# Optimization experiments

Measured on AMD Instinct MI355X. Metric: run time of the kernel, lower is better.

Reference implementation:

```python
import jax, jax.numpy as jnp
import numpy as np

D_MODEL = 512


def setup_inputs() -> dict:
    key = jax.random.key(0)
    ks = jax.random.split(key, 5)
    B, S, D = 4, 4096, D_MODEL
    scale = 1.0 / np.sqrt(D)
    return {
        "x": jax.random.normal(ks[0], (B, S, D), dtype=jnp.float32),
        "W_q": jax.random.normal(ks[1], (D, D), dtype=jnp.float32) * scale,
        "W_k": jax.random.normal(ks[2], (D, D), dtype=jnp.float32) * scale,
        "W_v": jax.random.normal(ks[3], (D, D), dtype=jnp.float32) * scale,
        "W_o": jax.random.normal(ks[4], (D, D), dtype=jnp.float32) * scale,
    }


def reference(x, W_q, W_k, W_v, W_o):
    # torch nn.Linear(d,d,bias=False): y = x @ W.T
    q = jnp.einsum("bsd,ed->bse", x, W_q)
    k = jnp.einsum("bsd,ed->bse", x, W_k)
    v = jnp.einsum("bsd,ed->bse", x, W_v)
    d_k = jnp.sqrt(jnp.asarray(D_MODEL, dtype=x.dtype))
    scores = jnp.einsum("bqd,bkd->bqk", q, k) / d_k  # [B,S,S]
    S = scores.shape[-1]
    causal = jnp.tril(jnp.ones((S, S), dtype=bool))  # True where allowed
    scores = jnp.where(causal, scores, -jnp.inf)
    attn = jax.nn.softmax(scores, axis=-1)
    context = jnp.einsum("bqk,bkd->bqd", attn, v)
    return jnp.einsum("bsd,ed->bse", context, W_o)
```

## Files before the change

### kernel.cpp

```cpp
#include <hip/hip_runtime.h>
#include <cstdint>

typedef __attribute__((ext_vector_type(8))) __bf16 bf16x8;
typedef __attribute__((ext_vector_type(4))) float f32x4;
typedef __attribute__((ext_vector_type(8))) unsigned short u16x8;

#define SEQ 4096
#define QKV_LD 1536

__device__ __forceinline__ unsigned short f2bf(float f) {
  unsigned u = __builtin_bit_cast(unsigned, f);
  u += 0x7fffu + ((u >> 16) & 1u);
  return (unsigned short)(u >> 16);
}

__device__ __forceinline__ float bf2f(unsigned short h) {
  return __builtin_bit_cast(float, (unsigned)h << 16);
}

__device__ __forceinline__ void async_copy16(const void* g, const void* lds) {
  __builtin_amdgcn_global_load_lds(
      (const __attribute__((address_space(1))) void*)(uintptr_t)g,
      (__attribute__((address_space(3))) void*)(unsigned)(uintptr_t)lds,
      16, 0, 0);
}

__global__ void cvt_bf16(const float* __restrict__ src, unsigned short* __restrict__ dst, int n) {
  int i = (blockIdx.x * 256 + threadIdx.x) * 4;
  if (i >= n) return;
  float4 v = *(const float4*)(src + i);
  ushort4 o;
  o.x = f2bf(v.x); o.y = f2bf(v.y); o.z = f2bf(v.z); o.w = f2bf(v.w);
  *(ushort4*)(dst + i) = o;
}

template <bool F32OUT>
__global__ __launch_bounds__(256, 2) void gemm_bt(
    const unsigned short* __restrict__ A, const unsigned short* __restrict__ B,
    void* __restrict__ C, int ldc)
{
  __shared__ unsigned short As[128 * 32];
  __shared__ unsigned short Bs[128 * 32];
  const int tid = threadIdx.x;
  const int lane = tid & 63;
  const int w = tid >> 6;
  const int l15 = lane & 15, quad = lane >> 4;
  const int wm = w & 1, wn = w >> 1;
  const long m0 = (long)blockIdx.x * 128;
  const long n0 = (long)blockIdx.y * 128;

  f32x4 acc[4][4] = {};

  for (int kt = 0; kt < 16; ++kt) {
    __syncthreads();
    {
      int c = tid;
      int row = c >> 2, chl = c & 3;
      int gch = (chl - (row >> 1)) & 3;
      async_copy16(A + (m0 + row) * 512 + kt * 32 + gch * 8, As + c * 8);
      async_copy16(B + (n0 + row) * 512 + kt * 32 + gch * 8, Bs + c * 8);
      c = tid + 256;
      row = c >> 2; chl = c & 3;
      gch = (chl - (row >> 1)) & 3;
      async_copy16(A + (m0 + row) * 512 + kt * 32 + gch * 8, As + c * 8);
      async_copy16(B + (n0 + row) * 512 + kt * 32 + gch * 8, Bs + c * 8);
    }
    __syncthreads();

    bf16x8 af[4], bfr[4];
#pragma unroll
    for (int mt = 0; mt < 4; ++mt) {
      int row = wm * 64 + mt * 16 + l15;
      int chl = (quad + (row >> 1)) & 3;
      af[mt] = *(const bf16x8*)(As + row * 32 + chl * 8);
    }
#pragma unroll
    for (int nt = 0; nt < 4; ++nt) {
      int row = wn * 64 + nt * 16 + l15;
      int chl = (quad + (row >> 1)) & 3;
      bfr[nt] = *(const bf16x8*)(Bs + row * 32 + chl * 8);
    }
#pragma unroll
    for (int mt = 0; mt < 4; ++mt)
#pragma unroll
      for (int nt = 0; nt < 4; ++nt)
        acc[mt][nt] = __builtin_amdgcn_mfma_f32_16x16x32_bf16(af[mt], bfr[nt], acc[mt][nt], 0, 0, 0);
  }

#pragma unroll
  for (int mt = 0; mt < 4; ++mt)
#pragma unroll
    for (int nt = 0; nt < 4; ++nt)
#pragma unroll
      for (int r = 0; r < 4; ++r) {
        long row = m0 + wm * 64 + mt * 16 + quad * 4 + r;
        long col = n0 + wn * 64 + nt * 16 + l15;
        float v = acc[mt][nt][r];
        if (F32OUT) ((float*)C)[row * ldc + col] = v;
        else        ((unsigned short*)C)[row * ldc + col] = f2bf(v);
      }
}

__global__ __launch_bounds__(256) void transpose_v(const unsigned short* __restrict__ QKV,
                                                   unsigned short* __restrict__ Vt)
{
  __shared__ unsigned short t[64 * 66];
  const int tid = threadIdx.x;
  const int b = blockIdx.z;
  const long s0 = (long)blockIdx.x * 64;
  const int d0 = blockIdx.y * 64;
#pragma unroll
  for (int i = 0; i < 2; ++i) {
    int c = tid + i * 256;
    int row = c >> 3, ch = c & 7;
    u16x8 v = *(const u16x8*)(QKV + ((long)b * SEQ + s0 + row) * QKV_LD + 1024 + d0 + ch * 8);
#pragma unroll
    for (int j = 0; j < 8; ++j) t[row * 66 + ch * 8 + j] = v[j];
  }
  __syncthreads();
#pragma unroll
  for (int i = 0; i < 2; ++i) {
    int c = tid + i * 256;
    int drow = c >> 3, sch = c & 7;
    u16x8 v;
#pragma unroll
    for (int j = 0; j < 8; ++j) v[j] = t[(sch * 8 + j) * 66 + drow];
    *(u16x8*)(Vt + ((long)b * 512 + d0 + drow) * SEQ + s0 + sch * 8) = v;
  }
}

__global__ __launch_bounds__(512, 2) void attn(const unsigned short* __restrict__ QKV,
                                               const unsigned short* __restrict__ Vt,
                                               unsigned short* __restrict__ part0,
                                               unsigned short* __restrict__ part1,
                                               unsigned short* __restrict__ part2,
                                               unsigned short* __restrict__ part3,
                                               float* __restrict__ mlbuf)
{
  extern __shared__ unsigned short smem[];
  unsigned short* Ps = smem + 65536;
  const int tid = threadIdx.x;
  const int lane = tid & 63, w = tid >> 6;
  const int l15 = lane & 15, quad = lane >> 4;

  const int f = blockIdx.x;
  const int xcd = f & 7;
  const int j = f >> 3;
  const int bat = xcd >> 1;
  const int half = xcd & 1;
  int qt, sv;
  if (j < 32) { qt = 31 - j; sv = 0; }
  else        { qt = 63 - j; sv = 1; }
  const int split = half * 2 + sv;

  const int q0 = qt * 128;
  const int wrow0 = q0 + w * 16;
  const float C1 = 0.04419417382415922f * 1.4426950408889634f;
  const float C2 = -12.0f * 1.4426950408889634f;

  bf16x8 qf[16];
  {
    const unsigned short* qp = QKV + ((long)bat * SEQ + wrow0 + l15) * QKV_LD;
#pragma unroll
    for (int dt = 0; dt < 16; ++dt)
      qf[dt] = *(const bf16x8*)(qp + dt * 32 + quad * 8);
  }
  f32x4 o[32] = {};
  f32x4 lacc = {0.f, 0.f, 0.f, 0.f};

  const int kt0 = split * (qt + 1);
  const int kt1 = kt0 + (qt + 1);

#define STAGE_KV(KT, BI)                                                               \
  {                                                                                    \
    unsigned short* Kb = smem + (BI) * 16384;                                          \
    unsigned short* Vb = smem + 32768 + (BI) * 16384;                                  \
    const int kk0 = (KT) * 32;                                                         \
    _Pragma("unroll")                                                                  \
    for (int i = 0; i < 4; ++i) {                                                      \
      int c = tid + i * 512;                                                           \
      int krow = c >> 6, chl = c & 63;                                                 \
      int gch = (chl & 56) | ((chl ^ krow) & 7);                                       \
      async_copy16(QKV + ((long)bat * SEQ + kk0 + krow) * QKV_LD + 512 + gch * 8,      \
                   Kb + c * 8);                                                        \
    }                                                                                  \
    _Pragma("unroll")                                                                  \
    for (int i = 0; i < 4; ++i) {                                                      \
      int c = tid + i * 512;                                                           \
      int d = c >> 2, chl = c & 3;                                                     \
      int gch = (chl - (d >> 1)) & 3;                                                  \
      async_copy16(Vt + ((long)bat * 512 + d) * SEQ + kk0 + gch * 8, Vb + c * 8);      \
    }                                                                                  \
  }

  STAGE_KV(kt0, 0);

  int bi = 0;
  for (int kt = kt0; kt < kt1; ++kt) {
    const int k0 = kt * 32;
    __syncthreads();

    if (kt + 1 < kt1) STAGE_KV(kt + 1, bi ^ 1);

    const unsigned short* Ks = smem + bi * 16384;
    const unsigned short* Vs = smem + 32768 + bi * 16384;

    const bool active = (k0 <= wrow0 + 15);
    if (active) {
      f32x4 s0v = {}, s1v = {};
#pragma unroll
      for (int dt = 0; dt < 16; ++dt) {
        int ch = dt * 4 + quad;
        {
          int krow = l15;
          int chl = (ch & 56) | ((ch ^ krow) & 7);
          bf16x8 kf = *(const bf16x8*)(Ks + krow * 512 + chl * 8);
          s0v = __builtin_amdgcn_mfma_f32_16x16x32_bf16(qf[dt], kf, s0v, 0, 0, 0);
        }
        {
          int krow = 16 + l15;
          int chl = (ch & 56) | ((ch ^ krow) & 7);
          bf16x8 kf = *(const bf16x8*)(Ks + krow * 512 + chl * 8);
          s1v = __builtin_amdgcn_mfma_f32_16x16x32_bf16(qf[dt], kf, s1v, 0, 0, 0);
        }
      }
      const bool diag = (k0 + 31 > wrow0);
#pragma unroll
      for (int r = 0; r < 4; ++r) {
        float e0 = exp2f(fmaf(s0v[r], C1, C2));
        float e1 = exp2f(fmaf(s1v[r], C1, C2));
        if (diag) {
          int qrow = wrow0 + quad * 4 + r;
          if (k0 + l15 > qrow) e0 = 0.f;
          if (k0 + 16 + l15 > qrow) e1 = 0.f;
        }
        lacc[r] += e0 + e1;
        Ps[w * 640 + (quad * 4 + r) * 40 + l15] = f2bf(e0);
        Ps[w * 640 + (quad * 4 + r) * 40 + 16 + l15] = f2bf(e1);
      }
      bf16x8 pf = *(const bf16x8*)(Ps + w * 640 + l15 * 40 + quad * 8);
#pragma unroll
      for (int t = 0; t < 32; ++t) {
        int d = t * 16 + l15;
        int chl = (quad + (d >> 1)) & 3;
        bf16x8 vf = *(const bf16x8*)(Vs + d * 32 + chl * 8);
        o[t] = __builtin_amdgcn_mfma_f32_16x16x32_bf16(pf, vf, o[t], 0, 0, 0);
      }
    }
    bi ^= 1;
  }
#undef STAGE_KV

  float lrow[4];
#pragma unroll
  for (int r = 0; r < 4; ++r) {
    float ps = lacc[r];
    ps += __shfl_xor(ps, 1);
    ps += __shfl_xor(ps, 2);
    ps += __shfl_xor(ps, 4);
    ps += __shfl_xor(ps, 8);
    lrow[r] = ps;
  }
  unsigned short* po = (split == 0) ? part0 : (split == 1) ? part1 : (split == 2) ? part2 : part3;
  float* mo = mlbuf + (long)split * 2 * 16384;
  float* lo = mo + 16384;
#pragma unroll
  for (int r = 0; r < 4; ++r) {
    float inv = lrow[r] > 0.f ? 1.0f / lrow[r] : 0.f;
    long row = (long)bat * SEQ + wrow0 + quad * 4 + r;
#pragma unroll
    for (int t = 0; t < 32; ++t)
      po[row * 512 + t * 16 + l15] = f2bf(o[t][r] * inv);
    if (l15 == 0) {
      mo[row] = 12.0f;
      lo[row] = lrow[r];
    }
  }
}

__global__ __launch_bounds__(256) void combine4(unsigned short* __restrict__ ctx,
                                                const unsigned short* __restrict__ part1,
                                                const unsigned short* __restrict__ part2,
                                                const unsigned short* __restrict__ part3,
                                                const float* __restrict__ mlbuf)
{
  const float L2E = 1.4426950408889634f;
  int t = blockIdx.x * 256 + threadIdx.x;
  int row = t >> 6;
  int c8 = (t & 63) * 8;
  float m0 = mlbuf[row],          l0 = mlbuf[16384 + row];
  float m1 = mlbuf[32768 + row],  l1 = mlbuf[49152 + row];
  float m2 = mlbuf[65536 + row],  l2 = mlbuf[81920 + row];
  float m3 = mlbuf[98304 + row],  l3 = mlbuf[114688 + row];
  float m = fmaxf(fmaxf(m0, m1), fmaxf(m2, m3));
  float w0 = l0 * exp2f((m0 - m) * L2E);
  float w1 = l1 * exp2f((m1 - m) * L2E);
  float w2 = l2 * exp2f((m2 - m) * L2E);
  float w3 = l3 * exp2f((m3 - m) * L2E);
  float inv = 1.0f / (w0 + w1 + w2 + w3);
  w0 *= inv; w1 *= inv; w2 *= inv; w3 *= inv;
  long off = (long)row * 512 + c8;
  u16x8 a = *(const u16x8*)(ctx + off);
  u16x8 bb = *(const u16x8*)(part1 + off);
  u16x8 cc = *(const u16x8*)(part2 + off);
  u16x8 dd = *(const u16x8*)(part3 + off);
  u16x8 o;
#pragma unroll
  for (int jj = 0; jj < 8; ++jj)
    o[jj] = f2bf(w0 * bf2f(a[jj]) + w1 * bf2f(bb[jj]) + w2 * bf2f(cc[jj]) + w3 * bf2f(dd[jj]));
  *(u16x8*)(ctx + off) = o;
}

extern "C" void kernel_launch(void* const* d_in, const int* in_sizes, int n_in,
                              void* d_out, int out_size, void* d_ws, size_t ws_size,
                              hipStream_t stream) {
  const float* x  = (const float*)d_in[0];
  const float* Wq = (const float*)d_in[1];
  const float* Wk = (const float*)d_in[2];
  const float* Wv = (const float*)d_in[3];
  const float* Wo = (const float*)d_in[4];
  float* out = (float*)d_out;

  char* ws = (char*)d_ws;
  unsigned short* xb   = (unsigned short*)(ws);
  unsigned short* wqkv = (unsigned short*)(ws + 16777216);
  unsigned short* wo   = (unsigned short*)(ws + 18350080);
  unsigned short* qkv  = (unsigned short*)(ws + 18874368);
  unsigned short* vt   = (unsigned short*)(ws + 69206016);
  unsigned short* ctx  = (unsigned short*)(ws + 85983232);
  unsigned short* part1 = xb;
  unsigned short* part2 = (unsigned short*)d_out;
  unsigned short* part3 = part2 + 8388608;
  float*          mlbuf = (float*)wqkv;

  (void)hipFuncSetAttribute((const void*)attn,
                            hipFuncAttributeMaxDynamicSharedMemorySize, 141312);

  cvt_bf16<<<8192, 256, 0, stream>>>(x, xb, 8388608);
  cvt_bf16<<<256, 256, 0, stream>>>(Wq, wqkv, 262144);
  cvt_bf16<<<256, 256, 0, stream>>>(Wk, wqkv + 262144, 262144);
  cvt_bf16<<<256, 256, 0, stream>>>(Wv, wqkv + 524288, 262144);
  cvt_bf16<<<256, 256, 0, stream>>>(Wo, wo, 262144);

  gemm_bt<false><<<dim3(128, 12), 256, 0, stream>>>(xb, wqkv, qkv, QKV_LD);
  transpose_v<<<dim3(64, 8, 4), 256, 0, stream>>>(qkv, vt);
  attn<<<dim3(512), 512, 141312, stream>>>(qkv, vt, ctx, part1, part2, part3, mlbuf);
  combine4<<<4096, 256, 0, stream>>>(ctx, part1, part2, part3, mlbuf);
  gemm_bt<true><<<dim3(128, 4), 256, 0, stream>>>(ctx, wo, out, 512);
}
```

Baseline: 288.2 us.

## Keep attention P tile in registers via swapped MFMA and permlane swaps

The QK^T MFMA operands are swapped so each lane holds scores transposed, which lets the softmax probabilities be packed to bf16 with v_cvt_pk_bf16_f32 and rearranged into the PV A-operand layout using permlane32/16 swaps instead of a round trip through LDS. This removes the per-tile LDS stores and reload of P along with the Ps buffer, shrinking dynamic shared memory from 141312 to 131072 bytes. The row-sum reduction is adjusted to the new layout, and s_setprio is raised around the MFMA loops to favour matrix issue. It relies on the permlane swap instructions and on the transposed layout mapping exactly onto the A operand.

```diff
diff --git a/kernel.cpp b/kernel.cpp
--- a/kernel.cpp
+++ b/kernel.cpp
@@ -23,6 +23,25 @@
       (const __attribute__((address_space(1))) void*)(uintptr_t)g,
       (__attribute__((address_space(3))) void*)(unsigned)(uintptr_t)lds,
       16, 0, 0);
+}
+
+__device__ __forceinline__ void pl32swap(unsigned& a, unsigned& b) {
+#if __has_builtin(__builtin_amdgcn_permlane32_swap)
+  typedef __attribute__((ext_vector_type(2))) unsigned u32x2;
+  u32x2 r = __builtin_amdgcn_permlane32_swap(a, b, false, false);
+  a = r[0]; b = r[1];
+#else
+  asm("v_permlane32_swap_b32 %0, %1" : "+v"(a), "+v"(b));
+#endif
+}
+__device__ __forceinline__ void pl16swap(unsigned& a, unsigned& b) {
+#if __has_builtin(__builtin_amdgcn_permlane16_swap)
+  typedef __attribute__((ext_vector_type(2))) unsigned u32x2;
+  u32x2 r = __builtin_amdgcn_permlane16_swap(a, b, false, false);
+  a = r[0]; b = r[1];
+#else
+  asm("v_permlane16_swap_b32 %0, %1" : "+v"(a), "+v"(b));
+#endif
 }
 
 __global__ void cvt_bf16(const float* __restrict__ src, unsigned short* __restrict__ dst, int n) {
@@ -138,7 +157,6 @@
                                                float* __restrict__ mlbuf)
 {
   extern __shared__ unsigned short smem[];
-  unsigned short* Ps = smem + 65536;
   const int tid = threadIdx.x;
   const int lane = tid & 63, w = tid >> 6;
   const int l15 = lane & 15, quad = lane >> 4;
@@ -166,7 +184,7 @@
       qf[dt] = *(const bf16x8*)(qp + dt * 32 + quad * 8);
   }
   f32x4 o[32] = {};
-  f32x4 lacc = {0.f, 0.f, 0.f, 0.f};
+  float lacc = 0.f;
 
   const int kt0 = split * (qt + 1);
   const int kt1 = kt0 + (qt + 1);
@@ -208,6 +226,7 @@
     const bool active = (k0 <= wrow0 + 15);
     if (active) {
       f32x4 s0v = {}, s1v = {};
+      __builtin_amdgcn_s_setprio(1);
 #pragma unroll
       for (int dt = 0; dt < 16; ++dt) {
         int ch = dt * 4 + quad;
@@ -215,30 +234,44 @@
           int krow = l15;
           int chl = (ch & 56) | ((ch ^ krow) & 7);
           bf16x8 kf = *(const bf16x8*)(Ks + krow * 512 + chl * 8);
-          s0v = __builtin_amdgcn_mfma_f32_16x16x32_bf16(qf[dt], kf, s0v, 0, 0, 0);
+          s0v = __builtin_amdgcn_mfma_f32_16x16x32_bf16(kf, qf[dt], s0v, 0, 0, 0);
         }
         {
           int krow = 16 + l15;
           int chl = (ch & 56) | ((ch ^ krow) & 7);
           bf16x8 kf = *(const bf16x8*)(Ks + krow * 512 + chl * 8);
-          s1v = __builtin_amdgcn_mfma_f32_16x16x32_bf16(qf[dt], kf, s1v, 0, 0, 0);
+          s1v = __builtin_amdgcn_mfma_f32_16x16x32_bf16(kf, qf[dt], s1v, 0, 0, 0);
         }
       }
+      __builtin_amdgcn_s_setprio(0);
+
       const bool diag = (k0 + 31 > wrow0);
+      const int qrow = wrow0 + l15;
+      float e0[4], e1[4];
 #pragma unroll
       for (int r = 0; r < 4; ++r) {
-        float e0 = exp2f(fmaf(s0v[r], C1, C2));
-        float e1 = exp2f(fmaf(s1v[r], C1, C2));
+        e0[r] = exp2f(fmaf(s0v[r], C1, C2));
+        e1[r] = exp2f(fmaf(s1v[r], C1, C2));
         if (diag) {
-          int qrow = wrow0 + quad * 4 + r;
-          if (k0 + l15 > qrow) e0 = 0.f;
-          if (k0 + 16 + l15 > qrow) e1 = 0.f;
+          if (k0 + quad * 4 + r > qrow) e0[r] = 0.f;
+          if (k0 + 16 + quad * 4 + r > qrow) e1[r] = 0.f;
         }
-        lacc[r] += e0 + e1;
-        Ps[w * 640 + (quad * 4 + r) * 40 + l15] = f2bf(e0);
-        Ps[w * 640 + (quad * 4 + r) * 40 + 16 + l15] = f2bf(e1);
+        lacc += e0[r] + e1[r];
       }
-      bf16x8 pf = *(const bf16x8*)(Ps + w * 640 + l15 * 40 + quad * 8);
+      unsigned pw0, pw1, pw2, pw3;
+      asm("v_cvt_pk_bf16_f32 %0, %1, %2" : "=v"(pw0) : "v"(e0[0]), "v"(e0[1]));
+      asm("v_cvt_pk_bf16_f32 %0, %1, %2" : "=v"(pw1) : "v"(e0[2]), "v"(e0[3]));
+      asm("v_cvt_pk_bf16_f32 %0, %1, %2" : "=v"(pw2) : "v"(e1[0]), "v"(e1[1]));
+      asm("v_cvt_pk_bf16_f32 %0, %1, %2" : "=v"(pw3) : "v"(e1[2]), "v"(e1[3]));
+      pl32swap(pw0, pw2);
+      pl32swap(pw1, pw3);
+      pl16swap(pw0, pw2);
+      pl16swap(pw1, pw3);
+      union { unsigned u[4]; bf16x8 v; } pu;
+      pu.u[0] = pw0; pu.u[1] = pw1; pu.u[2] = pw2; pu.u[3] = pw3;
+      bf16x8 pf = pu.v;
+
+      __builtin_amdgcn_s_setprio(1);
 #pragma unroll
       for (int t = 0; t < 32; ++t) {
         int d = t * 16 + l15;
@@ -246,21 +279,19 @@
         bf16x8 vf = *(const bf16x8*)(Vs + d * 32 + chl * 8);
         o[t] = __builtin_amdgcn_mfma_f32_16x16x32_bf16(pf, vf, o[t], 0, 0, 0);
       }
+      __builtin_amdgcn_s_setprio(0);
     }
     bi ^= 1;
   }
 #undef STAGE_KV
 
+  float ps = lacc;
+  ps += __shfl_xor(ps, 16);
+  ps += __shfl_xor(ps, 32);
   float lrow[4];
 #pragma unroll
-  for (int r = 0; r < 4; ++r) {
-    float ps = lacc[r];
-    ps += __shfl_xor(ps, 1);
-    ps += __shfl_xor(ps, 2);
-    ps += __shfl_xor(ps, 4);
-    ps += __shfl_xor(ps, 8);
-    lrow[r] = ps;
-  }
+  for (int r = 0; r < 4; ++r) lrow[r] = __shfl(ps, quad * 4 + r);
+
   unsigned short* po = (split == 0) ? part0 : (split == 1) ? part1 : (split == 2) ? part2 : part3;
   float* mo = mlbuf + (long)split * 2 * 16384;
   float* lo = mo + 16384;
@@ -334,7 +365,7 @@
   float*          mlbuf = (float*)wqkv;
 
   (void)hipFuncSetAttribute((const void*)attn,
-                            hipFuncAttributeMaxDynamicSharedMemorySize, 141312);
+                            hipFuncAttributeMaxDynamicSharedMemorySize, 131072);
 
   cvt_bf16<<<8192, 256, 0, stream>>>(x, xb, 8388608);
   cvt_bf16<<<256, 256, 0, stream>>>(Wq, wqkv, 262144);
@@ -344,7 +375,7 @@
 
   gemm_bt<false><<<dim3(128, 12), 256, 0, stream>>>(xb, wqkv, qkv, QKV_LD);
   transpose_v<<<dim3(64, 8, 4), 256, 0, stream>>>(qkv, vt);
-  attn<<<dim3(512), 512, 141312, stream>>>(qkv, vt, ctx, part1, part2, part3, mlbuf);
+  attn<<<dim3(512), 512, 131072, stream>>>(qkv, vt, ctx, part1, part2, part3, mlbuf);
   combine4<<<4096, 256, 0, stream>>>(ctx, part1, part2, part3, mlbuf);
   gemm_bt<true><<<dim3(128, 4), 256, 0, stream>>>(ctx, wo, out, 512);
 }
```

New measurement: 272.0 us. 5.6% less time.

## Use 32x32x16 MFMA in attention with permlane register-resident P operand

Applied to the files above, without the earlier changes.

Rewrites the attention kernel to use 32x32x16 bf16 MFMA with 4 waves of 32 query rows each, computing S transposed so that softmax probabilities can be packed with cvt_pk_bf16 and exchanged via permlane32_swap instead of going through LDS. This removes the P round-trip through shared memory and halves the K fragment reads per tile. In exchange, block size drops to 256 threads with one block per CU, accumulator and Q register pressure rise, and the row-sum reduction changes shape. It also merges the four weight conversion launches into one.

```diff
diff --git a/kernel.cpp b/kernel.cpp
--- a/kernel.cpp
+++ b/kernel.cpp
@@ -3,6 +3,7 @@
 
 typedef __attribute__((ext_vector_type(8))) __bf16 bf16x8;
 typedef __attribute__((ext_vector_type(4))) float f32x4;
+typedef __attribute__((ext_vector_type(16))) float f32x16;
 typedef __attribute__((ext_vector_type(8))) unsigned short u16x8;
 
 #define SEQ 4096
@@ -25,9 +26,32 @@
       16, 0, 0);
 }
 
+__device__ __forceinline__ void pl32swap(unsigned& a, unsigned& b) {
+#if __has_builtin(__builtin_amdgcn_permlane32_swap)
+  typedef __attribute__((ext_vector_type(2))) unsigned u32x2;
+  u32x2 r = __builtin_amdgcn_permlane32_swap(a, b, false, false);
+  a = r[0]; b = r[1];
+#else
+  asm("v_permlane32_swap_b32 %0, %1" : "+v"(a), "+v"(b));
+#endif
+}
+
 __global__ void cvt_bf16(const float* __restrict__ src, unsigned short* __restrict__ dst, int n) {
   int i = (blockIdx.x * 256 + threadIdx.x) * 4;
   if (i >= n) return;
+  float4 v = *(const float4*)(src + i);
+  ushort4 o;
+  o.x = f2bf(v.x); o.y = f2bf(v.y); o.z = f2bf(v.z); o.w = f2bf(v.w);
+  *(ushort4*)(dst + i) = o;
+}
+
+__global__ void cvt_w(const float* __restrict__ Wq, const float* __restrict__ Wk,
+                      const float* __restrict__ Wv, const float* __restrict__ Wo,
+                      unsigned short* __restrict__ wqkv, unsigned short* __restrict__ wo) {
+  int y = blockIdx.y;
+  const float* src = (y == 0) ? Wq : (y == 1) ? Wk : (y == 2) ? Wv : Wo;
+  unsigned short* dst = (y < 3) ? wqkv + y * 262144 : wo;
+  int i = (blockIdx.x * 256 + threadIdx.x) * 4;
   float4 v = *(const float4*)(src + i);
   ushort4 o;
   o.x = f2bf(v.x); o.y = f2bf(v.y); o.z = f2bf(v.z); o.w = f2bf(v.w);
@@ -129,7 +153,7 @@
   }
 }
 
-__global__ __launch_bounds__(512, 2) void attn(const unsigned short* __restrict__ QKV,
+__global__ __launch_bounds__(256, 1) void attn(const unsigned short* __restrict__ QKV,
                                                const unsigned short* __restrict__ Vt,
                                                unsigned short* __restrict__ part0,
                                                unsigned short* __restrict__ part1,
@@ -138,10 +162,9 @@
                                                float* __restrict__ mlbuf)
 {
   extern __shared__ unsigned short smem[];
-  unsigned short* Ps = smem + 65536;
   const int tid = threadIdx.x;
   const int lane = tid & 63, w = tid >> 6;
-  const int l15 = lane & 15, quad = lane >> 4;
+  const int l31 = lane & 31, h = lane >> 5;
 
   const int f = blockIdx.x;
   const int xcd = f & 7;
@@ -154,19 +177,19 @@
   const int split = half * 2 + sv;
 
   const int q0 = qt * 128;
-  const int wrow0 = q0 + w * 16;
+  const int wrow0 = q0 + w * 32;
   const float C1 = 0.04419417382415922f * 1.4426950408889634f;
   const float C2 = -12.0f * 1.4426950408889634f;
 
-  bf16x8 qf[16];
+  bf16x8 qf[32];
   {
-    const unsigned short* qp = QKV + ((long)bat * SEQ + wrow0 + l15) * QKV_LD;
-#pragma unroll
-    for (int dt = 0; dt < 16; ++dt)
-      qf[dt] = *(const bf16x8*)(qp + dt * 32 + quad * 8);
-  }
-  f32x4 o[32] = {};
-  f32x4 lacc = {0.f, 0.f, 0.f, 0.f};
+    const unsigned short* qp = QKV + ((long)bat * SEQ + wrow0 + l31) * QKV_LD;
+#pragma unroll
+    for (int c = 0; c < 32; ++c)
+      qf[c] = *(const bf16x8*)(qp + c * 16 + h * 8);
+  }
+  f32x16 o[16] = {};
+  float lacc = 0.f;
 
   const int kt0 = split * (qt + 1);
   const int kt1 = kt0 + (qt + 1);
@@ -177,16 +200,16 @@
     unsigned short* Vb = smem + 32768 + (BI) * 16384;                                  \
     const int kk0 = (KT) * 32;                                                         \
     _Pragma("unroll")                                                                  \
-    for (int i = 0; i < 4; ++i) {                                                      \
-      int c = tid + i * 512;                                                           \
+    for (int i = 0; i < 8; ++i) {                                                      \
+      int c = tid + i * 256;                                                           \
       int krow = c >> 6, chl = c & 63;                                                 \
       int gch = (chl & 56) | ((chl ^ krow) & 7);                                       \
       async_copy16(QKV + ((long)bat * SEQ + kk0 + krow) * QKV_LD + 512 + gch * 8,      \
                    Kb + c * 8);                                                        \
     }                                                                                  \
     _Pragma("unroll")                                                                  \
-    for (int i = 0; i < 4; ++i) {                                                      \
-      int c = tid + i * 512;                                                           \
+    for (int i = 0; i < 8; ++i) {                                                      \
+      int c = tid + i * 256;                                                           \
       int d = c >> 2, chl = c & 3;                                                     \
       int gch = (chl - (d >> 1)) & 3;                                                  \
       async_copy16(Vt + ((long)bat * 512 + d) * SEQ + kk0 + gch * 8, Vb + c * 8);      \
@@ -205,76 +228,81 @@
     const unsigned short* Ks = smem + bi * 16384;
     const unsigned short* Vs = smem + 32768 + bi * 16384;
 
-    const bool active = (k0 <= wrow0 + 15);
+    const bool active = (k0 <= wrow0 + 31);
     if (active) {
-      f32x4 s0v = {}, s1v = {};
-#pragma unroll
-      for (int dt = 0; dt < 16; ++dt) {
-        int ch = dt * 4 + quad;
-        {
-          int krow = l15;
-          int chl = (ch & 56) | ((ch ^ krow) & 7);
-          bf16x8 kf = *(const bf16x8*)(Ks + krow * 512 + chl * 8);
-          s0v = __builtin_amdgcn_mfma_f32_16x16x32_bf16(qf[dt], kf, s0v, 0, 0, 0);
-        }
-        {
-          int krow = 16 + l15;
-          int chl = (ch & 56) | ((ch ^ krow) & 7);
-          bf16x8 kf = *(const bf16x8*)(Ks + krow * 512 + chl * 8);
-          s1v = __builtin_amdgcn_mfma_f32_16x16x32_bf16(qf[dt], kf, s1v, 0, 0, 0);
-        }
+      f32x16 sacc = {};
+#pragma unroll
+      for (int c = 0; c < 32; ++c) {
+        int g = c * 2 + h;
+        int chl = (g & 56) | ((g ^ l31) & 7);
+        bf16x8 kf = *(const bf16x8*)(Ks + l31 * 512 + chl * 8);
+        sacc = __builtin_amdgcn_mfma_f32_32x32x16_bf16(kf, qf[c], sacc, 0, 0, 0);
       }
+
       const bool diag = (k0 + 31 > wrow0);
-#pragma unroll
-      for (int r = 0; r < 4; ++r) {
-        float e0 = exp2f(fmaf(s0v[r], C1, C2));
-        float e1 = exp2f(fmaf(s1v[r], C1, C2));
-        if (diag) {
-          int qrow = wrow0 + quad * 4 + r;
-          if (k0 + l15 > qrow) e0 = 0.f;
-          if (k0 + 16 + l15 > qrow) e1 = 0.f;
-        }
-        lacc[r] += e0 + e1;
-        Ps[w * 640 + (quad * 4 + r) * 40 + l15] = f2bf(e0);
-        Ps[w * 640 + (quad * 4 + r) * 40 + 16 + l15] = f2bf(e1);
+      const int qrow = wrow0 + l31;
+      float e[16];
+#pragma unroll
+      for (int r = 0; r < 16; ++r) {
+        int kl = (r & 3) + 8 * (r >> 2) + 4 * h;
+        float ev = exp2f(fmaf(sacc[r], C1, C2));
+        if (diag && (k0 + kl > qrow)) ev = 0.f;
+        e[r] = ev;
+        lacc += ev;
       }
-      bf16x8 pf = *(const bf16x8*)(Ps + w * 640 + l15 * 40 + quad * 8);
-#pragma unroll
-      for (int t = 0; t < 32; ++t) {
-        int d = t * 16 + l15;
-        int chl = (quad + (d >> 1)) & 3;
-        bf16x8 vf = *(const bf16x8*)(Vs + d * 32 + chl * 8);
-        o[t] = __builtin_amdgcn_mfma_f32_16x16x32_bf16(pf, vf, o[t], 0, 0, 0);
+      unsigned A0, A1, B0, B1, Cc0, Cc1, D0, D1;
+      asm("v_cvt_pk_bf16_f32 %0, %1, %2" : "=v"(A0) : "v"(e[0]), "v"(e[1]));
+      asm("v_cvt_pk_bf16_f32 %0, %1, %2" : "=v"(A1) : "v"(e[2]), "v"(e[3]));
+      asm("v_cvt_pk_bf16_f32 %0, %1, %2" : "=v"(B0) : "v"(e[4]), "v"(e[5]));
+      asm("v_cvt_pk_bf16_f32 %0, %1, %2" : "=v"(B1) : "v"(e[6]), "v"(e[7]));
+      asm("v_cvt_pk_bf16_f32 %0, %1, %2" : "=v"(Cc0) : "v"(e[8]), "v"(e[9]));
+      asm("v_cvt_pk_bf16_f32 %0, %1, %2" : "=v"(Cc1) : "v"(e[10]), "v"(e[11]));
+      asm("v_cvt_pk_bf16_f32 %0, %1, %2" : "=v"(D0) : "v"(e[12]), "v"(e[13]));
+      asm("v_cvt_pk_bf16_f32 %0, %1, %2" : "=v"(D1) : "v"(e[14]), "v"(e[15]));
+      pl32swap(A0, B0);
+      pl32swap(A1, B1);
+      pl32swap(Cc0, D0);
+      pl32swap(Cc1, D1);
+      union { unsigned u[4]; bf16x8 v; } p0, p1;
+      p0.u[0] = A0; p0.u[1] = A1; p0.u[2] = B0; p0.u[3] = B1;
+      p1.u[0] = Cc0; p1.u[1] = Cc1; p1.u[2] = D0; p1.u[3] = D1;
+      bf16x8 pa0 = p0.v, pa1 = p1.v;
+
+#pragma unroll
+      for (int t = 0; t < 16; ++t) {
+        int d = t * 32 + l31;
+        int g0 = (h + (d >> 1)) & 3;
+        bf16x8 vf0 = *(const bf16x8*)(Vs + d * 32 + g0 * 8);
+        o[t] = __builtin_amdgcn_mfma_f32_32x32x16_bf16(pa0, vf0, o[t], 0, 0, 0);
+        int g1 = (2 + h + (d >> 1)) & 3;
+        bf16x8 vf1 = *(const bf16x8*)(Vs + d * 32 + g1 * 8);
+        o[t] = __builtin_amdgcn_mfma_f32_32x32x16_bf16(pa1, vf1, o[t], 0, 0, 0);
       }
     }
     bi ^= 1;
   }
 #undef STAGE_KV
 
-  float lrow[4];
-#pragma unroll
-  for (int r = 0; r < 4; ++r) {
-    float ps = lacc[r];
-    ps += __shfl_xor(ps, 1);
-    ps += __shfl_xor(ps, 2);
-    ps += __shfl_xor(ps, 4);
-    ps += __shfl_xor(ps, 8);
-    lrow[r] = ps;
-  }
+  float ps = lacc;
+  ps += __shfl_xor(ps, 32);
+
   unsigned short* po = (split == 0) ? part0 : (split == 1) ? part1 : (split == 2) ? part2 : part3;
   float* mo = mlbuf + (long)split * 2 * 16384;
   float* lo = mo + 16384;
 #pragma unroll
-  for (int r = 0; r < 4; ++r) {
-    float inv = lrow[r] > 0.f ? 1.0f / lrow[r] : 0.f;
-    long row = (long)bat * SEQ + wrow0 + quad * 4 + r;
-#pragma unroll
-    for (int t = 0; t < 32; ++t)
-      po[row * 512 + t * 16 + l15] = f2bf(o[t][r] * inv);
-    if (l15 == 0) {
-      mo[row] = 12.0f;
-      lo[row] = lrow[r];
-    }
+  for (int r = 0; r < 16; ++r) {
+    int ql = (r & 3) + 8 * (r >> 2) + 4 * h;
+    float lv = __shfl(ps, ql);
+    float inv = lv > 0.f ? 1.0f / lv : 0.f;
+    long row = (long)bat * SEQ + wrow0 + ql;
+#pragma unroll
+    for (int t = 0; t < 16; ++t)
+      po[row * 512 + t * 32 + l31] = f2bf(o[t][r] * inv);
+  }
+  if (lane < 32) {
+    long row = (long)bat * SEQ + wrow0 + l31;
+    mo[row] = 12.0f;
+    lo[row] = ps;
   }
 }
 
@@ -334,17 +362,14 @@
   float*          mlbuf = (float*)wqkv;
 
   (void)hipFuncSetAttribute((const void*)attn,
-                            hipFuncAttributeMaxDynamicSharedMemorySize, 141312);
+                            hipFuncAttributeMaxDynamicSharedMemorySize, 131072);
 
   cvt_bf16<<<8192, 256, 0, stream>>>(x, xb, 8388608);
-  cvt_bf16<<<256, 256, 0, stream>>>(Wq, wqkv, 262144);
-  cvt_bf16<<<256, 256, 0, stream>>>(Wk, wqkv + 262144, 262144);
-  cvt_bf16<<<256, 256, 0, stream>>>(Wv, wqkv + 524288, 262144);
-  cvt_bf16<<<256, 256, 0, stream>>>(Wo, wo, 262144);
+  cvt_w<<<dim3(256, 4), 256, 0, stream>>>(Wq, Wk, Wv, Wo, wqkv, wo);
 
   gemm_bt<false><<<dim3(128, 12), 256, 0, stream>>>(xb, wqkv, qkv, QKV_LD);
   transpose_v<<<dim3(64, 8, 4), 256, 0, stream>>>(qkv, vt);
-  attn<<<dim3(512), 512, 141312, stream>>>(qkv, vt, ctx, part1, part2, part3, mlbuf);
+  attn<<<dim3(512), 256, 131072, stream>>>(qkv, vt, ctx, part1, part2, part3, mlbuf);
   combine4<<<4096, 256, 0, stream>>>(ctx, part1, part2, part3, mlbuf);
   gemm_bt<true><<<dim3(128, 4), 256, 0, stream>>>(ctx, wo, out, 512);
 }
```

New measurement: 1.100 ms. 282% more time.
